# Optimization experiments

Hardware: AMD Instinct MI355X
Metric: run time of the kernel (lower is better)

Reference implementation:

```python
import jax, jax.numpy as jnp
import numpy as np

EMBED_DIM = 1024
NUM_HEADS = 16
HEAD_DIM = EMBED_DIM // NUM_HEADS


def setup_inputs() -> dict:
    key = jax.random.key(0)
    ks = jax.random.split(key, 7)
    B, S, E = 8, 1024, EMBED_DIM
    # xavier-uniform-like scale for in_proj_weight [3E, E]
    bound_in = float(np.sqrt(6.0 / (3 * E + E)))
    bound_out = float(np.sqrt(6.0 / (E + E)))
    return {
        "q": jax.random.normal(ks[0], (B, S, E), jnp.float32),
        "k": jax.random.normal(ks[1], (B, S, E), jnp.float32),
        "v": jax.random.normal(ks[2], (B, S, E), jnp.float32),
        "in_proj_weight": jax.random.uniform(ks[3], (3 * E, E), jnp.float32, -bound_in, bound_in),
        "in_proj_bias": jnp.zeros((3 * E,), jnp.float32),
        "out_proj_weight": jax.random.uniform(ks[4], (E, E), jnp.float32, -bound_out, bound_out),
        "out_proj_bias": jnp.zeros((E,), jnp.float32),
    }


def reference(q, k, v, in_proj_weight, in_proj_bias, out_proj_weight, out_proj_bias):
    B, S, E = q.shape
    H, D = NUM_HEADS, HEAD_DIM
    w_q, w_k, w_v = jnp.split(in_proj_weight, 3, axis=0)
    b_q, b_k, b_v = jnp.split(in_proj_bias, 3, axis=0)
    # packed in-projection: linear(x, W, b) = x @ W.T + b
    qp = q @ w_q.T + b_q
    kp = k @ w_k.T + b_k
    vp = v @ w_v.T + b_v
    # [B, S, E] -> [B, H, S, D]
    qh = qp.reshape(B, S, H, D).transpose(0, 2, 1, 3)
    kh = kp.reshape(B, S, H, D).transpose(0, 2, 1, 3)
    vh = vp.reshape(B, S, H, D).transpose(0, 2, 1, 3)
    scale = D ** -0.5
    # explicit full attention in fp32 (matches original fp32 cast path)
    scores = jnp.einsum("bhqd,bhkd->bhqk", qh, kh) * scale
    attn = jax.nn.softmax(scores, axis=-1)
    ctx = jnp.einsum("bhqk,bhkd->bhqd", attn, vh)  # [B, H, S, D]
    ctx = ctx.transpose(0, 2, 1, 3).reshape(B, S, E)
    out = ctx @ out_proj_weight.T + out_proj_bias
    return out
```

## Files before the change

### kernel.cpp

```cpp
#include <hip/hip_runtime.h>
#include <stdint.h>

#define TOK 8192
#define EDIM 1024
#define NH 16
#define HD 64
#define SEQ 1024
#define BATCH 8

typedef short bf16x8 __attribute__((ext_vector_type(8)));
typedef short bf16x4 __attribute__((ext_vector_type(4)));
typedef float f32x4 __attribute__((ext_vector_type(4)));
typedef float f32x16 __attribute__((ext_vector_type(16)));
typedef unsigned int u32x2 __attribute__((ext_vector_type(2)));
typedef unsigned int u32x4 __attribute__((ext_vector_type(4)));

__device__ __forceinline__ short f2bf(float f) {
  union { float f; uint32_t u; } c; c.f = f;
  uint32_t u = c.u;
  u += 0x7FFFu + ((u >> 16) & 1u);
  return (short)(u >> 16);
}
__device__ __forceinline__ float bf2f(short h) {
  union { uint32_t u; float f; } c; c.u = ((uint32_t)(uint16_t)h) << 16;
  return c.f;
}
__device__ __forceinline__ uint32_t bfr(float f) {
  union { float f; uint32_t u; } c; c.f = f;
  return (c.u + 0x8000u) >> 16;
}
__device__ __forceinline__ uint32_t cvtpk(float lo, float hi_) {
  uint32_t r;
  asm("v_cvt_pk_bf16_f32 %0, %1, %2" : "=v"(r) : "v"(lo), "v"(hi_));
  return r;
}

#define GLDS16(ldsp, gp) __builtin_amdgcn_global_load_lds( \
    (__attribute__((address_space(1))) void*)(gp),          \
    (__attribute__((address_space(3))) void*)(ldsp), 16, 0, 0)

__global__ __launch_bounds__(256) void cast_all(
    const float* __restrict__ q, const float* __restrict__ k,
    const float* __restrict__ v, const float* __restrict__ wi,
    const float* __restrict__ wo, short* __restrict__ dst) {
  const size_t NTOK = (size_t)TOK * EDIM;
  const size_t NWI = 3u * EDIM * EDIM;
  size_t i = ((size_t)blockIdx.x * 256 + threadIdx.x) * 4;
  const float* src;
  if (i < NTOK) src = q + i;
  else if (i < 2 * NTOK) src = k + (i - NTOK);
  else if (i < 3 * NTOK) src = v + (i - 2 * NTOK);
  else if (i < 3 * NTOK + NWI) src = wi + (i - 3 * NTOK);
  else src = wo + (i - 3 * NTOK - NWI);
  float4 f = *(const float4*)src;
  bf16x4 o;
  o[0] = f2bf(f.x); o[1] = f2bf(f.y); o[2] = f2bf(f.z); o[3] = f2bf(f.w);
  *(bf16x4*)(dst + i) = o;
}

#define GEMM_TILE9(KT, BUF, VMC, DOSTAGE)                                      \
  {                                                                            \
    asm volatile("s_waitcnt vmcnt(" VMC ")" ::: "memory");                     \
    __builtin_amdgcn_s_barrier();                                              \
    const short* Ab = lds + (BUF) * 12288;                                     \
    const short* Bb = Ab + 8192;                                               \
    bf16x8 af[4], bv[4];                                                       \
    _Pragma("unroll")                                                          \
    for (int mi = 0; mi < 4; mi++)                                             \
      af[mi] = *(const bf16x8*)&Ab[(wrBase + mi * 16 + fr) * 32 + fgsw * 8];   \
    _Pragma("unroll")                                                          \
    for (int ni = 0; ni < 4; ni++)                                             \
      bv[ni] = *(const bf16x8*)&Bb[(wcBase + ni * 16 + fr) * 32 + fgsw * 8];   \
    if (DOSTAGE) {                                                             \
      char* d_ = (char*)lds + (((BUF) + 2) % 3) * 24576 + t * 16;              \
      GLDS16(d_,         aS + ((KT) + 2) * 32);                                \
      GLDS16(d_ + 8192,  aS + ((KT) + 2) * 32 + 128 * 1024);                   \
      GLDS16(d_ + 16384, bS + ((KT) + 2) * 32);                                \
    }                                                                          \
    __builtin_amdgcn_s_setprio(1);                                             \
    _Pragma("unroll")                                                          \
    for (int mi = 0; mi < 4; mi++) {                                           \
      _Pragma("unroll")                                                        \
      for (int ni = 0; ni < 4; ni++)                                           \
        acc[mi][ni] = __builtin_amdgcn_mfma_f32_16x16x32_bf16(                 \
            af[mi], bv[ni], acc[mi][ni], 0, 0, 0);                             \
    }                                                                          \
    __builtin_amdgcn_s_setprio(0);                                             \
  }

template<int MODE>
__global__ __launch_bounds__(512, 4)
void gemm_bt9(const short* __restrict__ Abase, const short* __restrict__ Wbase,
              const float* __restrict__ biasBase, void* __restrict__ outv) {
  __shared__ short lds[36864];

  const int z = (MODE == 0) ? blockIdx.z : 0;
  const size_t NTOK = (size_t)TOK * EDIM;
  const short* A  = Abase + (size_t)z * NTOK;
  const short* Bw = Wbase + (size_t)z * EDIM * EDIM;
  const float* bias = biasBase + z * EDIM;

  const int t = threadIdx.x;
  const int l = t & 63, w = t >> 6;
  const int fr = l & 15, fg = l >> 4;
  const int fgsw = fg ^ ((fr >> 1) & 3);
  const int wrBase = (w >> 1) * 64;
  const int wcBase = (w & 1) * 64;
  const int rowBase = blockIdx.x * 256;
  const int colBase = blockIdx.y * 128;

  f32x4 acc[4][4];
#pragma unroll
  for (int i = 0; i < 4; i++)
#pragma unroll
    for (int j = 0; j < 4; j++) acc[i][j] = (f32x4){0.f, 0.f, 0.f, 0.f};

  const int sChunk = (t & 3) ^ ((t >> 3) & 3);
  const short* aS = A  + (size_t)(rowBase + (t >> 2)) * EDIM + sChunk * 8;
  const short* bS = Bw + (size_t)(colBase + (t >> 2)) * EDIM + sChunk * 8;

#pragma unroll
  for (int s = 0; s < 2; s++) {
    char* d = (char*)lds + s * 24576 + t * 16;
    GLDS16(d,         aS + s * 32);
    GLDS16(d + 8192,  aS + s * 32 + 128 * 1024);
    GLDS16(d + 16384, bS + s * 32);
  }

#pragma unroll 1
  for (int kt = 0; kt < 30; kt += 3) {
    GEMM_TILE9(kt,     0, "3", true);
    GEMM_TILE9(kt + 1, 1, "3", true);
    GEMM_TILE9(kt + 2, 2, "3", (kt + 2 <= 29));
  }
  GEMM_TILE9(30, 0, "3", false);
  GEMM_TILE9(31, 1, "0", false);

  if (MODE == 0 && z == 2) {
    __syncthreads();
#pragma unroll
    for (int mi = 0; mi < 4; mi++)
#pragma unroll
      for (int ni = 0; ni < 4; ni++) {
        int dloc = wcBase + ni * 16 + fr;
        int sl = wrBase + mi * 16 + fg * 4;
        float b0 = bias[colBase + dloc];
        u32x2 pk;
        pk[0] = cvtpk(acc[mi][ni][0] + b0, acc[mi][ni][1] + b0);
        pk[1] = cvtpk(acc[mi][ni][2] + b0, acc[mi][ni][3] + b0);
        int byteoff = dloc * 512 + (((sl >> 3) ^ (dloc & 31)) << 4) + ((fg & 1) << 3);
        *(u32x2*)((char*)lds + byteoff) = pk;
      }
    __syncthreads();
    short* outp = (short*)outv + 2 * NTOK;
    const int b_ = rowBase >> 10;
    const int s0 = rowBase & 1023;
#pragma unroll
    for (int i = 0; i < 8; i++) {
      int id = i * 512 + t;
      int dloc = id >> 5, c = id & 31;
      bf16x8 vv = *(const bf16x8*)((char*)lds + dloc * 512 + ((c ^ (dloc & 31)) << 4));
      int gcol = colBase + dloc;
      int h_ = gcol >> 6, d_ = gcol & 63;
      *(bf16x8*)(outp + ((((size_t)((b_ * NH + h_) * HD + d_)) << 10) | (s0 + c * 8))) = vv;
    }
  } else {
#pragma unroll
    for (int mi = 0; mi < 4; mi++)
#pragma unroll
      for (int ni = 0; ni < 4; ni++)
#pragma unroll
        for (int r = 0; r < 4; r++) {
          int grow = rowBase + wrBase + mi * 16 + fg * 4 + r;
          int gcol = colBase + wcBase + ni * 16 + fr;
          float v = acc[mi][ni][r] + bias[gcol];
          if (MODE == 0) {
            int b_ = grow >> 10, s_ = grow & 1023;
            int h_ = gcol >> 6,  d_ = gcol & 63;
            short* outp = (short*)outv + (size_t)z * NTOK;
            outp[((size_t)((b_ * NH + h_) * SEQ + s_) << 6) | d_] = f2bf(v);
          } else {
            ((float*)outv)[(size_t)grow * EDIM + gcol] = v;
          }
        }
  }
}

__global__ __launch_bounds__(512)
void attn_fwd14(const short* __restrict__ proj, short* __restrict__ ctx) {
  __shared__ short lds[16384];

  const int t = threadIdx.x;
  const int l = t & 63, w = t >> 6;
  const int ln = l & 31, hi = l >> 5;

  const int n = blockIdx.x + 4 * (blockIdx.y + 16 * blockIdx.z);
  const int qt = (n >> 3) & 3;
  const int hl = (n & 7) | ((n >> 5) << 3);
  const int h = hl & 15, b = hl >> 4;

  const size_t NTOK = (size_t)TOK * EDIM;
  const size_t headOff = (size_t)(b * NH + h) * SEQ * HD;
  const short* Qp  = proj + headOff;
  const short* Kp  = proj + NTOK + headOff;
  const short* VpT = proj + 2 * NTOK + headOff;

  const int q0 = qt * 256;
  const int qrow = q0 + w * 32 + ln;

  const int sRow = t >> 3;
  const int sColSw = ((t & 7) ^ (sRow & 7)) << 3;
  const short* Ksrc0 = Kp  + (size_t)sRow * HD  + sColSw;
  const short* Vsrc0 = VpT + (size_t)sRow * SEQ + sColSw;

  const float qscale = 0.18033688011112042f;
  bf16x8 bQ[4];
#pragma unroll
  for (int ds = 0; ds < 4; ds++) {
    bf16x8 v = *(const bf16x8*)(Qp + (size_t)qrow * HD + ds * 16 + hi * 8);
#pragma unroll
    for (int j = 0; j < 8; j++) v[j] = (short)bfr(bf2f(v[j]) * qscale);
    bQ[ds] = v;
  }

  f32x16 ot[2], lsum;
#pragma unroll
  for (int i = 0; i < 16; i++) { ot[0][i] = 0.f; ot[1][i] = 0.f; lsum[i] = 0.f; }
  f32x16 z16 = {};
  bf16x8 ones;
#pragma unroll
  for (int j = 0; j < 8; j++) ones[j] = (short)0x3F80;

  GLDS16((char*)lds + t * 16,        Ksrc0);
  GLDS16((char*)lds + 8192 + t * 16, Vsrc0);
  __syncthreads();

  for (int jt = 0; jt < SEQ / 64; jt++) {
    const int bufByte = (jt & 1) << 14;
    const int nb = bufByte ^ (1 << 14);

    if (jt + 1 < SEQ / 64) {
      GLDS16((char*)lds + nb + t * 16,        Ksrc0 + (size_t)(jt + 1) * 64 * HD);
      GLDS16((char*)lds + nb + 8192 + t * 16, Vsrc0 + (jt + 1) * 64);
    }

    f32x16 sa[2];
    __builtin_amdgcn_s_setprio(1);
#pragma unroll
    for (int kvb = 0; kvb < 2; kvb++) {
      int kv = kvb * 32 + ln;
      bf16x8 aK0 = *(const bf16x8*)((const char*)lds + bufByte + kv * 128 +
                                    ((hi ^ (kv & 7)) << 4));
      sa[kvb] = __builtin_amdgcn_mfma_f32_32x32x16_bf16(aK0, bQ[0], z16, 0, 0, 0);
#pragma unroll
      for (int ds = 1; ds < 4; ds++) {
        bf16x8 aK = *(const bf16x8*)((const char*)lds + bufByte + kv * 128 +
                                     (((ds * 2 + hi) ^ (kv & 7)) << 4));
        sa[kvb] = __builtin_amdgcn_mfma_f32_32x32x16_bf16(aK, bQ[ds], sa[kvb], 0, 0, 0);
      }
    }
    __builtin_amdgcn_s_setprio(0);

#pragma unroll
    for (int i = 0; i < 16; i++) {
      sa[0][i] = exp2f(sa[0][i]);
      sa[1][i] = exp2f(sa[1][i]);
    }

    bf16x8 pa[4];
#pragma unroll
    for (int ks = 0; ks < 4; ks++) {
      const int kvb = ks >> 1, hf = (ks & 1) * 8;
      uint32_t A1 = cvtpk(sa[kvb][hf + 0], sa[kvb][hf + 1]);
      uint32_t A2 = cvtpk(sa[kvb][hf + 2], sa[kvb][hf + 3]);
      uint32_t B1 = cvtpk(sa[kvb][hf + 4], sa[kvb][hf + 5]);
      uint32_t B2 = cvtpk(sa[kvb][hf + 6], sa[kvb][hf + 7]);
      u32x4 wds;
#if __has_builtin(__builtin_amdgcn_permlane32_swap)
      u32x2 r13 = __builtin_amdgcn_permlane32_swap(A1, B1, false, false);
      u32x2 r24 = __builtin_amdgcn_permlane32_swap(A2, B2, false, false);
      wds[0] = r13[0]; wds[2] = r13[1];
      wds[1] = r24[0]; wds[3] = r24[1];
#else
      uint32_t send1 = hi ? A1 : B1;
      uint32_t send2 = hi ? A2 : B2;
      uint32_t recv1 = (uint32_t)__shfl_xor((int)send1, 32);
      uint32_t recv2 = (uint32_t)__shfl_xor((int)send2, 32);
      wds[0] = hi ? recv1 : A1;
      wds[1] = hi ? recv2 : A2;
      wds[2] = hi ? B1 : recv1;
      wds[3] = hi ? B2 : recv2;
#endif
      pa[ks] = __builtin_bit_cast(bf16x8, wds);
    }

    const char* VtB = (const char*)lds + bufByte + 8192;
    __builtin_amdgcn_s_setprio(1);
#pragma unroll
    for (int ks = 0; ks < 4; ks++) {
#pragma unroll
      for (int dblk = 0; dblk < 2; dblk++) {
        int d = dblk * 32 + ln;
        bf16x8 aV = *(const bf16x8*)(VtB + d * 128 + (((ks * 2 + hi) ^ (d & 7)) << 4));
        ot[dblk] = __builtin_amdgcn_mfma_f32_32x32x16_bf16(aV, pa[ks], ot[dblk], 0, 0, 0);
      }
      lsum = __builtin_amdgcn_mfma_f32_32x32x16_bf16(ones, pa[ks], lsum, 0, 0, 0);
    }
    __builtin_amdgcn_s_setprio(0);

    __syncthreads();
  }

  float rl = 1.0f / lsum[0];

#pragma unroll
  for (int dblk = 0; dblk < 2; dblk++)
#pragma unroll
    for (int r = 0; r < 16; r++) {
      int d = dblk * 32 + (r & 3) + 8 * (r >> 2) + 4 * hi;
      int qrl = w * 32 + ln;
      int byteoff = qrl * 128 + (((d >> 3) ^ (qrl & 7)) << 4) + (d & 7) * 2;
      *(short*)((char*)lds + byteoff) = (short)bfr(ot[dblk][r] * rl);
    }
  __syncthreads();
#pragma unroll
  for (int i = 0; i < 4; i++) {
    int chunk = t * 4 + i;
    int row = chunk >> 3, c8 = chunk & 7;
    bf16x8 vv = *(const bf16x8*)((const char*)lds + row * 128 + ((c8 ^ (row & 7)) << 4));
    *(bf16x8*)(ctx + (size_t)(b * SEQ + q0 + row) * EDIM + h * HD + c8 * 8) = vv;
  }
}

extern "C" void kernel_launch(void* const* d_in, const int* in_sizes, int n_in,
                              void* d_out, int out_size, void* d_ws, size_t ws_size,
                              hipStream_t stream) {
  const float* q  = (const float*)d_in[0];
  const float* k  = (const float*)d_in[1];
  const float* v  = (const float*)d_in[2];
  const float* wi = (const float*)d_in[3];
  const float* bi = (const float*)d_in[4];
  const float* wo = (const float*)d_in[5];
  const float* bo = (const float*)d_in[6];
  float* out = (float*)d_out;

  short* ws = (short*)d_ws;
  const size_t NTOK = (size_t)TOK * EDIM;
  short* qkv_bf   = ws;
  short* w_in_bf  = qkv_bf + 3 * NTOK;
  short* w_out_bf = w_in_bf + 3 * (size_t)EDIM * EDIM;
  short* proj_bf  = w_out_bf + (size_t)EDIM * EDIM;
  short* ctx_bf   = qkv_bf;

  const size_t totalCast = 3 * NTOK + 3 * (size_t)EDIM * EDIM + (size_t)EDIM * EDIM;
  cast_all<<<dim3((unsigned)(totalCast / 4 / 256)), 256, 0, stream>>>(q, k, v, wi, wo, qkv_bf);

  gemm_bt9<0><<<dim3(TOK / 256, EDIM / 128, 3), 512, 0, stream>>>(qkv_bf, w_in_bf, bi, proj_bf);
  attn_fwd14<<<dim3(SEQ / 256, NH, BATCH), 512, 0, stream>>>(proj_bf, ctx_bf);
  gemm_bt9<1><<<dim3(TOK / 256, EDIM / 128, 1), 512, 0, stream>>>(ctx_bf, w_out_bf, bo, out);
}
```

Before: 153.4 us.

## Fuse fp32-to-bf16 activation cast into the QKV projection GEMM

Removes the separate cast pass over the q/k/v activations. The QKV GEMM now loads fp32 A tiles into registers, converts them with v_cvt_pk_bf16_f32, and writes them to LDS. The weights still use global_load_lds after a smaller weight-only cast kernel. This saves a full read/write pass over the activations. In exchange, each block re-reads fp32 A (twice the bytes), the register pressure and pipeline are more complex, and wait counts are hand-tuned. The output GEMM is split into its own non-templated kernel.

```diff
diff --git a/kernel.cpp b/kernel.cpp
--- a/kernel.cpp
+++ b/kernel.cpp
@@ -39,30 +39,24 @@
     (__attribute__((address_space(1))) void*)(gp),          \
     (__attribute__((address_space(3))) void*)(ldsp), 16, 0, 0)
 
-__global__ __launch_bounds__(256) void cast_all(
-    const float* __restrict__ q, const float* __restrict__ k,
-    const float* __restrict__ v, const float* __restrict__ wi,
-    const float* __restrict__ wo, short* __restrict__ dst) {
-  const size_t NTOK = (size_t)TOK * EDIM;
+__global__ __launch_bounds__(256) void cast_w(
+    const float* __restrict__ wi, const float* __restrict__ wo,
+    short* __restrict__ dst) {
   const size_t NWI = 3u * EDIM * EDIM;
   size_t i = ((size_t)blockIdx.x * 256 + threadIdx.x) * 4;
-  const float* src;
-  if (i < NTOK) src = q + i;
-  else if (i < 2 * NTOK) src = k + (i - NTOK);
-  else if (i < 3 * NTOK) src = v + (i - 2 * NTOK);
-  else if (i < 3 * NTOK + NWI) src = wi + (i - 3 * NTOK);
-  else src = wo + (i - 3 * NTOK - NWI);
+  const float* src = (i < NWI) ? wi + i : wo + (i - NWI);
   float4 f = *(const float4*)src;
   bf16x4 o;
   o[0] = f2bf(f.x); o[1] = f2bf(f.y); o[2] = f2bf(f.z); o[3] = f2bf(f.w);
   *(bf16x4*)(dst + i) = o;
 }
 
-#define GEMM_TILE9(KT, BUF, VMC, DOSTAGE)                                      \
+#define QKV_TILE(KT, BUFI, K1S, DOSTAGE, DOWRITE)                              \
   {                                                                            \
-    asm volatile("s_waitcnt vmcnt(" VMC ")" ::: "memory");                     \
+    asm volatile("s_waitcnt vmcnt(" K1S ") lgkmcnt(0)" ::: "memory");          \
     __builtin_amdgcn_s_barrier();                                              \
-    const short* Ab = lds + (BUF) * 12288;                                     \
+    const int bi_ = (BUFI);                                                    \
+    const short* Ab = lds + bi_ * 12288;                                       \
     const short* Bb = Ab + 8192;                                               \
     bf16x8 af[4], bv[4];                                                       \
     _Pragma("unroll")                                                          \
@@ -72,10 +66,13 @@
     for (int ni = 0; ni < 4; ni++)                                             \
       bv[ni] = *(const bf16x8*)&Bb[(wcBase + ni * 16 + fr) * 32 + fgsw * 8];   \
     if (DOSTAGE) {                                                             \
-      char* d_ = (char*)lds + (((BUF) + 2) % 3) * 24576 + t * 16;              \
-      GLDS16(d_,         aS + ((KT) + 2) * 32);                                \
-      GLDS16(d_ + 8192,  aS + ((KT) + 2) * 32 + 128 * 1024);                   \
-      GLDS16(d_ + 16384, bS + ((KT) + 2) * 32);                                \
+      const float* as_ = aF + ((KT) + 2) * 32;                                 \
+      nA0 = *(const float4*)(as_);                                             \
+      nA1 = *(const float4*)(as_ + 4);                                         \
+      nA2 = *(const float4*)(as_ + 131072);                                    \
+      nA3 = *(const float4*)(as_ + 131072 + 4);                                \
+      int b2_ = bi_ + 2; if (b2_ >= 3) b2_ -= 3;                               \
+      GLDS16((char*)lds + b2_ * 24576 + 16384 + t * 16, bS + ((KT) + 2) * 32); \
     }                                                                          \
     __builtin_amdgcn_s_setprio(1);                                             \
     _Pragma("unroll")                                                          \
@@ -86,17 +83,29 @@
             af[mi], bv[ni], acc[mi][ni], 0, 0, 0);                             \
     }                                                                          \
     __builtin_amdgcn_s_setprio(0);                                             \
-  }
-
-template<int MODE>
+    if (DOWRITE) {                                                             \
+      int b1_ = bi_ + 1; if (b1_ >= 3) b1_ -= 3;                               \
+      char* wb = (char*)lds + b1_ * 24576;                                     \
+      u32x4 w1, w2;                                                            \
+      w1[0] = cvtpk(pA0.x, pA0.y); w1[1] = cvtpk(pA0.z, pA0.w);                \
+      w1[2] = cvtpk(pA1.x, pA1.y); w1[3] = cvtpk(pA1.z, pA1.w);                \
+      w2[0] = cvtpk(pA2.x, pA2.y); w2[1] = cvtpk(pA2.z, pA2.w);                \
+      w2[2] = cvtpk(pA3.x, pA3.y); w2[3] = cvtpk(pA3.z, pA3.w);                \
+      *(u32x4*)(wb + t * 16) = w1;                                             \
+      *(u32x4*)(wb + 8192 + t * 16) = w2;                                      \
+    }                                                                          \
+    if (DOSTAGE) { pA0 = nA0; pA1 = nA1; pA2 = nA2; pA3 = nA3; }               \
+  }
+
 __global__ __launch_bounds__(512, 4)
-void gemm_bt9(const short* __restrict__ Abase, const short* __restrict__ Wbase,
-              const float* __restrict__ biasBase, void* __restrict__ outv) {
+void gemm_qkv(const float* __restrict__ qf, const float* __restrict__ kf,
+              const float* __restrict__ vf, const short* __restrict__ Wbase,
+              const float* __restrict__ biasBase, short* __restrict__ outp0) {
   __shared__ short lds[36864];
 
-  const int z = (MODE == 0) ? blockIdx.z : 0;
+  const int z = blockIdx.z;
   const size_t NTOK = (size_t)TOK * EDIM;
-  const short* A  = Abase + (size_t)z * NTOK;
+  const float* Af = (z == 0) ? qf : (z == 1) ? kf : vf;
   const short* Bw = Wbase + (size_t)z * EDIM * EDIM;
   const float* bias = biasBase + z * EDIM;
 
@@ -116,27 +125,50 @@
     for (int j = 0; j < 4; j++) acc[i][j] = (f32x4){0.f, 0.f, 0.f, 0.f};
 
   const int sChunk = (t & 3) ^ ((t >> 3) & 3);
-  const short* aS = A  + (size_t)(rowBase + (t >> 2)) * EDIM + sChunk * 8;
+  const float* aF = Af + (size_t)(rowBase + (t >> 2)) * EDIM + sChunk * 8;
   const short* bS = Bw + (size_t)(colBase + (t >> 2)) * EDIM + sChunk * 8;
 
-#pragma unroll
-  for (int s = 0; s < 2; s++) {
-    char* d = (char*)lds + s * 24576 + t * 16;
-    GLDS16(d,         aS + s * 32);
-    GLDS16(d + 8192,  aS + s * 32 + 128 * 1024);
-    GLDS16(d + 16384, bS + s * 32);
-  }
-
+  float4 pA0, pA1, pA2, pA3, nA0, nA1, nA2, nA3;
+
+  {
+    pA0 = *(const float4*)(aF);
+    pA1 = *(const float4*)(aF + 4);
+    pA2 = *(const float4*)(aF + 131072);
+    pA3 = *(const float4*)(aF + 131072 + 4);
+    GLDS16((char*)lds + 16384 + t * 16, bS);
+    nA0 = *(const float4*)(aF + 32);
+    nA1 = *(const float4*)(aF + 36);
+    nA2 = *(const float4*)(aF + 131072 + 32);
+    nA3 = *(const float4*)(aF + 131072 + 36);
+    GLDS16((char*)lds + 24576 + 16384 + t * 16, bS + 32);
+    u32x4 w1, w2;
+    w1[0] = cvtpk(pA0.x, pA0.y); w1[1] = cvtpk(pA0.z, pA0.w);
+    w1[2] = cvtpk(pA1.x, pA1.y); w1[3] = cvtpk(pA1.z, pA1.w);
+    w2[0] = cvtpk(pA2.x, pA2.y); w2[1] = cvtpk(pA2.z, pA2.w);
+    w2[2] = cvtpk(pA3.x, pA3.y); w2[3] = cvtpk(pA3.z, pA3.w);
+    *(u32x4*)((char*)lds + t * 16) = w1;
+    *(u32x4*)((char*)lds + 8192 + t * 16) = w2;
+    w1[0] = cvtpk(nA0.x, nA0.y); w1[1] = cvtpk(nA0.z, nA0.w);
+    w1[2] = cvtpk(nA1.x, nA1.y); w1[3] = cvtpk(nA1.z, nA1.w);
+    w2[0] = cvtpk(nA2.x, nA2.y); w2[1] = cvtpk(nA2.z, nA2.w);
+    w2[2] = cvtpk(nA3.x, nA3.y); w2[3] = cvtpk(nA3.z, nA3.w);
+    *(u32x4*)((char*)lds + 24576 + t * 16) = w1;
+    *(u32x4*)((char*)lds + 24576 + 8192 + t * 16) = w2;
+  }
+
+  QKV_TILE(0, 0, "1", true, false);
+  {
+    int bcur = 1;
 #pragma unroll 1
-  for (int kt = 0; kt < 30; kt += 3) {
-    GEMM_TILE9(kt,     0, "3", true);
-    GEMM_TILE9(kt + 1, 1, "3", true);
-    GEMM_TILE9(kt + 2, 2, "3", (kt + 2 <= 29));
-  }
-  GEMM_TILE9(30, 0, "3", false);
-  GEMM_TILE9(31, 1, "0", false);
-
-  if (MODE == 0 && z == 2) {
+    for (int kt = 1; kt <= 29; kt++) {
+      QKV_TILE(kt, bcur, "5", true, true);
+      bcur = (bcur == 2) ? 0 : bcur + 1;
+    }
+  }
+  QKV_TILE(30, 0, "5", false, true);
+  QKV_TILE(31, 1, "0", false, false);
+
+  if (z == 2) {
     __syncthreads();
 #pragma unroll
     for (int mi = 0; mi < 4; mi++)
@@ -152,7 +184,7 @@
         *(u32x2*)((char*)lds + byteoff) = pk;
       }
     __syncthreads();
-    short* outp = (short*)outv + 2 * NTOK;
+    short* outp = outp0 + 2 * NTOK;
     const int b_ = rowBase >> 10;
     const int s0 = rowBase & 1023;
 #pragma unroll
@@ -174,16 +206,95 @@
           int grow = rowBase + wrBase + mi * 16 + fg * 4 + r;
           int gcol = colBase + wcBase + ni * 16 + fr;
           float v = acc[mi][ni][r] + bias[gcol];
-          if (MODE == 0) {
-            int b_ = grow >> 10, s_ = grow & 1023;
-            int h_ = gcol >> 6,  d_ = gcol & 63;
-            short* outp = (short*)outv + (size_t)z * NTOK;
-            outp[((size_t)((b_ * NH + h_) * SEQ + s_) << 6) | d_] = f2bf(v);
-          } else {
-            ((float*)outv)[(size_t)grow * EDIM + gcol] = v;
-          }
+          int b_ = grow >> 10, s_ = grow & 1023;
+          int h_ = gcol >> 6,  d_ = gcol & 63;
+          short* outp = outp0 + (size_t)z * NTOK;
+          outp[((size_t)((b_ * NH + h_) * SEQ + s_) << 6) | d_] = f2bf(v);
         }
   }
+}
+
+#define GEMM_TILE9(KT, BUF, VMC, DOSTAGE)                                      \
+  {                                                                            \
+    asm volatile("s_waitcnt vmcnt(" VMC ")" ::: "memory");                     \
+    __builtin_amdgcn_s_barrier();                                              \
+    const short* Ab = lds + (BUF) * 12288;                                     \
+    const short* Bb = Ab + 8192;                                               \
+    bf16x8 af[4], bv[4];                                                       \
+    _Pragma("unroll")                                                          \
+    for (int mi = 0; mi < 4; mi++)                                             \
+      af[mi] = *(const bf16x8*)&Ab[(wrBase + mi * 16 + fr) * 32 + fgsw * 8];   \
+    _Pragma("unroll")                                                          \
+    for (int ni = 0; ni < 4; ni++)                                             \
+      bv[ni] = *(const bf16x8*)&Bb[(wcBase + ni * 16 + fr) * 32 + fgsw * 8];   \
+    if (DOSTAGE) {                                                             \
+      char* d_ = (char*)lds + (((BUF) + 2) % 3) * 24576 + t * 16;              \
+      GLDS16(d_,         aS + ((KT) + 2) * 32);                                \
+      GLDS16(d_ + 8192,  aS + ((KT) + 2) * 32 + 128 * 1024);                   \
+      GLDS16(d_ + 16384, bS + ((KT) + 2) * 32);                                \
+    }                                                                          \
+    __builtin_amdgcn_s_setprio(1);                                             \
+    _Pragma("unroll")                                                          \
+    for (int mi = 0; mi < 4; mi++) {                                           \
+      _Pragma("unroll")                                                        \
+      for (int ni = 0; ni < 4; ni++)                                           \
+        acc[mi][ni] = __builtin_amdgcn_mfma_f32_16x16x32_bf16(                 \
+            af[mi], bv[ni], acc[mi][ni], 0, 0, 0);                             \
+    }                                                                          \
+    __builtin_amdgcn_s_setprio(0);                                             \
+  }
+
+__global__ __launch_bounds__(512, 4)
+void gemm_out(const short* __restrict__ A, const short* __restrict__ Bw,
+              const float* __restrict__ bias, float* __restrict__ outf) {
+  __shared__ short lds[36864];
+
+  const int t = threadIdx.x;
+  const int l = t & 63, w = t >> 6;
+  const int fr = l & 15, fg = l >> 4;
+  const int fgsw = fg ^ ((fr >> 1) & 3);
+  const int wrBase = (w >> 1) * 64;
+  const int wcBase = (w & 1) * 64;
+  const int rowBase = blockIdx.x * 256;
+  const int colBase = blockIdx.y * 128;
+
+  f32x4 acc[4][4];
+#pragma unroll
+  for (int i = 0; i < 4; i++)
+#pragma unroll
+    for (int j = 0; j < 4; j++) acc[i][j] = (f32x4){0.f, 0.f, 0.f, 0.f};
+
+  const int sChunk = (t & 3) ^ ((t >> 3) & 3);
+  const short* aS = A  + (size_t)(rowBase + (t >> 2)) * EDIM + sChunk * 8;
+  const short* bS = Bw + (size_t)(colBase + (t >> 2)) * EDIM + sChunk * 8;
+
+#pragma unroll
+  for (int s = 0; s < 2; s++) {
+    char* d = (char*)lds + s * 24576 + t * 16;
+    GLDS16(d,         aS + s * 32);
+    GLDS16(d + 8192,  aS + s * 32 + 128 * 1024);
+    GLDS16(d + 16384, bS + s * 32);
+  }
+
+#pragma unroll 1
+  for (int kt = 0; kt < 30; kt += 3) {
+    GEMM_TILE9(kt,     0, "3", true);
+    GEMM_TILE9(kt + 1, 1, "3", true);
+    GEMM_TILE9(kt + 2, 2, "3", (kt + 2 <= 29));
+  }
+  GEMM_TILE9(30, 0, "3", false);
+  GEMM_TILE9(31, 1, "0", false);
+
+#pragma unroll
+  for (int mi = 0; mi < 4; mi++)
+#pragma unroll
+    for (int ni = 0; ni < 4; ni++)
+#pragma unroll
+      for (int r = 0; r < 4; r++) {
+        int grow = rowBase + wrBase + mi * 16 + fg * 4 + r;
+        int gcol = colBase + wcBase + ni * 16 + fr;
+        outf[(size_t)grow * EDIM + gcol] = acc[mi][ni][r] + bias[gcol];
+      }
 }
 
 __global__ __launch_bounds__(512)
@@ -346,16 +457,14 @@
 
   short* ws = (short*)d_ws;
   const size_t NTOK = (size_t)TOK * EDIM;
-  short* qkv_bf   = ws;
-  short* w_in_bf  = qkv_bf + 3 * NTOK;
+  short* ctx_bf   = ws;
+  short* w_in_bf  = ctx_bf + 3 * NTOK;
   short* w_out_bf = w_in_bf + 3 * (size_t)EDIM * EDIM;
   short* proj_bf  = w_out_bf + (size_t)EDIM * EDIM;
-  short* ctx_bf   = qkv_bf;
-
-  const size_t totalCast = 3 * NTOK + 3 * (size_t)EDIM * EDIM + (size_t)EDIM * EDIM;
-  cast_all<<<dim3((unsigned)(totalCast / 4 / 256)), 256, 0, stream>>>(q, k, v, wi, wo, qkv_bf);
-
-  gemm_bt9<0><<<dim3(TOK / 256, EDIM / 128, 3), 512, 0, stream>>>(qkv_bf, w_in_bf, bi, proj_bf);
+
+  cast_w<<<dim3(4 * EDIM * EDIM / 4 / 256), 256, 0, stream>>>(wi, wo, w_in_bf);
+
+  gemm_qkv<<<dim3(TOK / 256, EDIM / 128, 3), 512, 0, stream>>>(q, k, v, w_in_bf, bi, proj_bf);
   attn_fwd14<<<dim3(SEQ / 256, NH, BATCH), 512, 0, stream>>>(proj_bf, ctx_bf);
-  gemm_bt9<1><<<dim3(TOK / 256, EDIM / 128, 1), 512, 0, stream>>>(ctx_bf, w_out_bf, bo, out);
-}
+  gemm_out<<<dim3(TOK / 256, EDIM / 128), 512, 0, stream>>>(ctx_bf, w_out_bf, bo, out);
+}
```

After: 265.2 us. 1.73x slower.
